# Kernel tuning notes

Hardware: AMD Instinct MI355X
Metric: run time of the kernel (lower is better)

## Reference

```python
import jax, jax.numpy as jnp
import numpy as np
from functools import partial

B, T, H, K = 64, 256, 200, 48
START_TAG, END_TAG = 46, 47


def setup_inputs() -> dict:
    key = jax.random.key(0)
    k1, k2, k3 = jax.random.split(key, 3)
    feats = jax.random.normal(k1, (B, T, H), dtype=jnp.float32)
    W_e = jax.random.normal(k2, (K, H), dtype=jnp.float32) * (6.0 / (K + H)) ** 0.5
    b_e = jnp.zeros((K,), dtype=jnp.float32)
    targets = jax.random.randint(k3, (B, T), 0, K * K, dtype=jnp.int64)
    mask = jnp.ones((B, T), dtype=jnp.int32)
    return {"feats": feats, "W_e": W_e, "b_e": b_e, "targets": targets,
            "mask": mask, "start_tag": START_TAG, "end_tag": END_TAG}


def reference(feats, W_e, b_e, targets, mask, start_tag, end_tag):
    # feats: [B,T,H]; emission: [B,T,K]
    emission = jnp.einsum('bth,kh->btk', feats, W_e) + b_e
    Bs, Ts, Ks = emission.shape
    lengths = mask.sum(-1)  # [B]
    valid = jnp.arange(Ts)[None, :] < lengths[:, None]  # [B,T]

    # crf_scores[b,t,i,j] = emission[b,t,j] (unsqueeze(2).expand). Gather at
    # flattened index targets = i*K + j picks emission[b,t, targets % K].
    gold_per_t = jnp.take_along_axis(emission, (targets % Ks)[..., None], axis=2)[..., 0]
    gold_score = jnp.sum(jnp.where(valid, gold_per_t, 0.0), axis=1)  # [B]

    # Forward algorithm. t=0: scores_upto_t = scores[:,0,start_tag,:] = emission[:,0,:]
    s0 = jnp.where((lengths > 0)[:, None], emission[:, 0, :], 0.0)  # [B,K]

    def step(s, xs):
        em_t, active = xs  # em_t: [B,K], active: [B]
        # scores[b,t,i,j] + s[b,i], logsumexp over i (prev tag)
        new = jax.scipy.special.logsumexp(em_t[:, None, :] + s[:, :, None], axis=1)
        s = jnp.where(active[:, None], new, s)
        return s, None

    xs = (jnp.swapaxes(emission[:, 1:, :], 0, 1), jnp.swapaxes(valid[:, 1:], 0, 1))
    s_final, _ = jax.lax.scan(step, s0, xs)

    all_paths_scores = s_final[:, end_tag]  # [B]
    viterbi_loss = all_paths_scores - gold_score
    return viterbi_loss
```

## Files before the change

kernel.cpp:

```cpp
#include <hip/hip_runtime.h>

#define BB 64
#define TT 256
#define HH 200
#define KK 48
#define C4 50
#define TPB 16
#define FS4 51

__global__ __launch_bounds__(256, 4)
void crf_fused_kernel(const float* __restrict__ feats,
                      const float* __restrict__ W_e,
                      const float* __restrict__ b_e,
                      const int*   __restrict__ targets,
                      const int*   __restrict__ mask,
                      const int*   __restrict__ end_tag_p,
                      float*       __restrict__ out)
{
    __shared__ float4 f_lds[TPB * FS4];
    __shared__ float  m_arr[4][TPB], s_arr[4][TPB];
    __shared__ float  g_arr[4][TPB], e_arr[4][TPB];

    const int tid  = threadIdx.x;
    const int lane = tid & 63;
    const int w    = tid >> 6;
    const int bidx = blockIdx.x >> 4;
    const int tq   = blockIdx.x & 15;

    const float4* feats4 = reinterpret_cast<const float4*>(feats) +
                           (size_t)(bidx * TT + tq * TPB) * C4;
    for (int i = tid; i < TPB * C4; i += 256) {
        const int r = i / C4, c = i - r * C4;
        f_lds[r * FS4 + c] = feats4[i];
    }

    int len;
    {
        const int4 mv4 = reinterpret_cast<const int4*>(mask + bidx * TT)[lane];
        int mv = mv4.x + mv4.y + mv4.z + mv4.w;
        #pragma unroll
        for (int off = 32; off >= 1; off >>= 1) mv += __shfl_xor(mv, off);
        len = mv;
    }
    __syncthreads();

    const int t_loc  = lane & 15;
    const int kg     = lane >> 4;
    const int k0     = w * 12 + kg * 3;
    const int t_glob = tq * TPB + t_loc;

    const float4* W4   = reinterpret_cast<const float4*>(W_e);
    const float4* wp0  = W4 + (size_t)(k0 + 0) * C4;
    const float4* wp1  = W4 + (size_t)(k0 + 1) * C4;
    const float4* wp2  = W4 + (size_t)(k0 + 2) * C4;
    const float4* frow = &f_lds[t_loc * FS4];

    float a0 = b_e[k0], a1 = b_e[k0 + 1], a2 = b_e[k0 + 2];
    #pragma unroll 2
    for (int c = 0; c < C4; ++c) {
        const float4 f  = frow[c];
        const float4 w0 = wp0[c];
        const float4 w1 = wp1[c];
        const float4 w2 = wp2[c];
        a0 = fmaf(f.x,w0.x, fmaf(f.y,w0.y, fmaf(f.z,w0.z, fmaf(f.w,w0.w, a0))));
        a1 = fmaf(f.x,w1.x, fmaf(f.y,w1.y, fmaf(f.z,w1.z, fmaf(f.w,w1.w, a1))));
        a2 = fmaf(f.x,w2.x, fmaf(f.y,w2.y, fmaf(f.z,w2.z, fmaf(f.w,w2.w, a2))));
    }

    const int ET  = end_tag_p[0];
    const int tgt = targets[bidx * TT + t_glob] % KK;

    float m = fmaxf(fmaxf(a0, a1), a2);
    float s = expf(a0 - m) + expf(a1 - m) + expf(a2 - m);
    float g = ((k0     == tgt) ? a0 : 0.0f)
            + ((k0 + 1 == tgt) ? a1 : 0.0f)
            + ((k0 + 2 == tgt) ? a2 : 0.0f);
    float e = ((k0     == ET) ? a0 : 0.0f)
            + ((k0 + 1 == ET) ? a1 : 0.0f)
            + ((k0 + 2 == ET) ? a2 : 0.0f);

    #pragma unroll
    for (int off = 16; off <= 32; off <<= 1) {
        const float om = __shfl_xor(m, off);
        const float os = __shfl_xor(s, off);
        const float nm = fmaxf(m, om);
        s = s * expf(m - nm) + os * expf(om - nm);
        m = nm;
        g += __shfl_xor(g, off);
        e += __shfl_xor(e, off);
    }
    if (lane < TPB) {
        m_arr[w][t_loc] = m; s_arr[w][t_loc] = s;
        g_arr[w][t_loc] = g; e_arr[w][t_loc] = e;
    }
    __syncthreads();

    if (tid < TPB) {
        const int t = tid;
        float M = m_arr[0][t], S = s_arr[0][t];
        #pragma unroll
        for (int i2 = 1; i2 < 4; ++i2) {
            const float om = m_arr[i2][t], os = s_arr[i2][t];
            const float nm = fmaxf(M, om);
            S = S * expf(M - nm) + os * expf(om - nm);
            M = nm;
        }
        const float lse  = M + logf(S);
        const float gold = g_arr[0][t] + g_arr[1][t] + g_arr[2][t] + g_arr[3][t];
        const float eend = e_arr[0][t] + e_arr[1][t] + e_arr[2][t] + e_arr[3][t];
        const int gt = tq * TPB + t;

        float c = 0.0f;
        if (gt < len)          c -= gold;
        if (gt == len - 1)     c += eend;
        else if (gt < len - 1) c += lse;

        #pragma unroll
        for (int off = 8; off >= 1; off >>= 1) c += __shfl_xor(c, off);
        if (t == 0) atomicAdd(out + bidx, c);
    }
}

extern "C" void kernel_launch(void* const* d_in, const int* in_sizes, int n_in,
                              void* d_out, int out_size, void* d_ws, size_t ws_size,
                              hipStream_t stream) {
    const float* feats   = (const float*)d_in[0];
    const float* W_e     = (const float*)d_in[1];
    const float* b_e     = (const float*)d_in[2];
    const int*   targets = (const int*)d_in[3];
    const int*   mask    = (const int*)d_in[4];
    const int*   et      = (const int*)d_in[6];
    float*       out     = (float*)d_out;

    hipMemsetAsync(out, 0, BB * sizeof(float), stream);
    crf_fused_kernel<<<dim3(BB * (TT / TPB)), dim3(256), 0, stream>>>(
        feats, W_e, b_e, targets, mask, et, out);
}
```

Measured before the change: 94.30 us.

## Compute emission GEMM with bf16 MFMA and 64-timestep tiles per block

Replaces the per-thread fp32 FMA dot products with bf16 16x16x32 MFMA instructions. Feats and W_e are converted to bf16 into LDS, and each block now handles 64 timesteps instead of 16, so there are 256 blocks instead of 1024. The log-sum-exp, gold-score and end-tag reductions are done with in-wave shuffles over the MFMA output layout, with one atomic per block. This targets the FMA throughput and the repeated W_e global reads, at the cost of bf16 precision in the emissions and fewer blocks to fill the GPU.

```diff
diff --git a/kernel.cpp b/kernel.cpp
--- a/kernel.cpp
+++ b/kernel.cpp
@@ -1,37 +1,56 @@
 #include <hip/hip_runtime.h>
+#include <hip/hip_bf16.h>
 
 #define BB 64
 #define TT 256
 #define HH 200
 #define KK 48
 #define C4 50
-#define TPB 16
-#define FS4 51
+#define AS 216
 
-__global__ __launch_bounds__(256, 4)
-void crf_fused_kernel(const float* __restrict__ feats,
-                      const float* __restrict__ W_e,
-                      const float* __restrict__ b_e,
-                      const int*   __restrict__ targets,
-                      const int*   __restrict__ mask,
-                      const int*   __restrict__ end_tag_p,
-                      float*       __restrict__ out)
+typedef __attribute__((ext_vector_type(8))) short bf16x8;
+typedef __attribute__((ext_vector_type(4))) float f32x4;
+
+static __device__ __forceinline__ unsigned short f2bf(float x) {
+    __hip_bfloat16 h = __float2bfloat16(x);
+    return *reinterpret_cast<unsigned short*>(&h);
+}
+
+__global__ __launch_bounds__(256)
+void crf_mfma_kernel(const float* __restrict__ feats,
+                     const float* __restrict__ W_e,
+                     const float* __restrict__ b_e,
+                     const int*   __restrict__ targets,
+                     const int*   __restrict__ mask,
+                     const int*   __restrict__ end_tag_p,
+                     float*       __restrict__ out)
 {
-    __shared__ float4 f_lds[TPB * FS4];
-    __shared__ float  m_arr[4][TPB], s_arr[4][TPB];
-    __shared__ float  g_arr[4][TPB], e_arr[4][TPB];
+    __shared__ __align__(16) unsigned short Albs[64 * AS];
+    __shared__ __align__(16) unsigned short Wlds[48 * AS];
+    __shared__ float wpart[4];
 
     const int tid  = threadIdx.x;
     const int lane = tid & 63;
     const int w    = tid >> 6;
-    const int bidx = blockIdx.x >> 4;
-    const int tq   = blockIdx.x & 15;
+    const int bidx = blockIdx.x >> 2;
+    const int tq   = blockIdx.x & 3;
 
-    const float4* feats4 = reinterpret_cast<const float4*>(feats) +
-                           (size_t)(bidx * TT + tq * TPB) * C4;
-    for (int i = tid; i < TPB * C4; i += 256) {
-        const int r = i / C4, c = i - r * C4;
-        f_lds[r * FS4 + c] = feats4[i];
+    {
+        const float4* f4 = reinterpret_cast<const float4*>(feats) +
+                           (size_t)(bidx * TT + tq * 64) * C4;
+        for (int i = tid; i < 64 * C4; i += 256) {
+            const int r = i / C4, cc = i - r * C4;
+            const float4 v = f4[i];
+            ushort4 o = { f2bf(v.x), f2bf(v.y), f2bf(v.z), f2bf(v.w) };
+            *reinterpret_cast<ushort4*>(&Albs[r * AS + cc * 4]) = o;
+        }
+        const float4* w4 = reinterpret_cast<const float4*>(W_e);
+        for (int i = tid; i < KK * C4; i += 256) {
+            const int r = i / C4, cc = i - r * C4;
+            const float4 v = w4[i];
+            ushort4 o = { f2bf(v.x), f2bf(v.y), f2bf(v.z), f2bf(v.w) };
+            *reinterpret_cast<ushort4*>(&Wlds[r * AS + cc * 4]) = o;
+        }
     }
 
     int len;
@@ -44,80 +63,79 @@
     }
     __syncthreads();
 
-    const int t_loc  = lane & 15;
-    const int kg     = lane >> 4;
-    const int k0     = w * 12 + kg * 3;
-    const int t_glob = tq * TPB + t_loc;
+    const int rg = lane >> 4;
+    const int cc = lane & 15;
 
-    const float4* W4   = reinterpret_cast<const float4*>(W_e);
-    const float4* wp0  = W4 + (size_t)(k0 + 0) * C4;
-    const float4* wp1  = W4 + (size_t)(k0 + 1) * C4;
-    const float4* wp2  = W4 + (size_t)(k0 + 2) * C4;
-    const float4* frow = &f_lds[t_loc * FS4];
+    const unsigned short* Ap  = &Albs[(w * 16 + cc) * AS];
+    const unsigned short* Bp0 = &Wlds[(0  + cc) * AS];
+    const unsigned short* Bp1 = &Wlds[(16 + cc) * AS];
+    const unsigned short* Bp2 = &Wlds[(32 + cc) * AS];
 
-    float a0 = b_e[k0], a1 = b_e[k0 + 1], a2 = b_e[k0 + 2];
-    #pragma unroll 2
-    for (int c = 0; c < C4; ++c) {
-        const float4 f  = frow[c];
-        const float4 w0 = wp0[c];
-        const float4 w1 = wp1[c];
-        const float4 w2 = wp2[c];
-        a0 = fmaf(f.x,w0.x, fmaf(f.y,w0.y, fmaf(f.z,w0.z, fmaf(f.w,w0.w, a0))));
-        a1 = fmaf(f.x,w1.x, fmaf(f.y,w1.y, fmaf(f.z,w1.z, fmaf(f.w,w1.w, a1))));
-        a2 = fmaf(f.x,w2.x, fmaf(f.y,w2.y, fmaf(f.z,w2.z, fmaf(f.w,w2.w, a2))));
+    f32x4 ac0 = {0.f, 0.f, 0.f, 0.f};
+    f32x4 ac1 = {0.f, 0.f, 0.f, 0.f};
+    f32x4 ac2 = {0.f, 0.f, 0.f, 0.f};
+
+    #pragma unroll
+    for (int kc = 0; kc < 7; ++kc) {
+        const int koff = kc * 32 + rg * 8;
+        bf16x8 a, b0, b1, b2;
+        if (kc < 6 || rg == 0) {
+            a  = *reinterpret_cast<const bf16x8*>(Ap  + koff);
+            b0 = *reinterpret_cast<const bf16x8*>(Bp0 + koff);
+            b1 = *reinterpret_cast<const bf16x8*>(Bp1 + koff);
+            b2 = *reinterpret_cast<const bf16x8*>(Bp2 + koff);
+        } else {
+            a = (bf16x8)(short)0; b0 = a; b1 = a; b2 = a;
+        }
+        ac0 = __builtin_amdgcn_mfma_f32_16x16x32_bf16(a, b0, ac0, 0, 0, 0);
+        ac1 = __builtin_amdgcn_mfma_f32_16x16x32_bf16(a, b1, ac1, 0, 0, 0);
+        ac2 = __builtin_amdgcn_mfma_f32_16x16x32_bf16(a, b2, ac2, 0, 0, 0);
     }
 
-    const int ET  = end_tag_p[0];
-    const int tgt = targets[bidx * TT + t_glob] % KK;
+    const float bb0 = b_e[cc], bb1 = b_e[16 + cc], bb2 = b_e[32 + cc];
+    const int   ET  = end_tag_p[0];
 
-    float m = fmaxf(fmaxf(a0, a1), a2);
-    float s = expf(a0 - m) + expf(a1 - m) + expf(a2 - m);
-    float g = ((k0     == tgt) ? a0 : 0.0f)
-            + ((k0 + 1 == tgt) ? a1 : 0.0f)
-            + ((k0 + 2 == tgt) ? a2 : 0.0f);
-    float e = ((k0     == ET) ? a0 : 0.0f)
-            + ((k0 + 1 == ET) ? a1 : 0.0f)
-            + ((k0 + 2 == ET) ? a2 : 0.0f);
+    float csum = 0.0f;
+    #pragma unroll
+    for (int j = 0; j < 4; ++j) {
+        const float x0 = ac0[j] + bb0;
+        const float x1 = ac1[j] + bb1;
+        const float x2 = ac2[j] + bb2;
 
-    #pragma unroll
-    for (int off = 16; off <= 32; off <<= 1) {
-        const float om = __shfl_xor(m, off);
-        const float os = __shfl_xor(s, off);
-        const float nm = fmaxf(m, om);
-        s = s * expf(m - nm) + os * expf(om - nm);
-        m = nm;
-        g += __shfl_xor(g, off);
-        e += __shfl_xor(e, off);
+        const int r  = w * 16 + rg * 4 + j;
+        const int gt = tq * 64 + r;
+        const int tg = targets[bidx * TT + gt] % KK;
+
+        float mx = fmaxf(fmaxf(x0, x1), x2);
+        #pragma unroll
+        for (int off = 8; off >= 1; off >>= 1) mx = fmaxf(mx, __shfl_xor(mx, off));
+        float s = expf(x0 - mx) + expf(x1 - mx) + expf(x2 - mx);
+        float g = ((0  + cc) == tg ? x0 : 0.f) + ((16 + cc) == tg ? x1 : 0.f)
+                + ((32 + cc) == tg ? x2 : 0.f);
+        float e = ((0  + cc) == ET ? x0 : 0.f) + ((16 + cc) == ET ? x1 : 0.f)
+                + ((32 + cc) == ET ? x2 : 0.f);
+        #pragma unroll
+        for (int off = 8; off >= 1; off >>= 1) {
+            s += __shfl_xor(s, off);
+            g += __shfl_xor(g, off);
+            e += __shfl_xor(e, off);
+        }
+        const float lse = mx + logf(s);
+
+        float cr = 0.0f;
+        if (gt < len)          cr -= g;
+        if (gt == len - 1)     cr += e;
+        else if (gt < len - 1) cr += lse;
+        csum += cr;
     }
-    if (lane < TPB) {
-        m_arr[w][t_loc] = m; s_arr[w][t_loc] = s;
-        g_arr[w][t_loc] = g; e_arr[w][t_loc] = e;
-    }
+
+    float v = (cc == 0) ? csum : 0.0f;
+    v += __shfl_xor(v, 16);
+    v += __shfl_xor(v, 32);
+    if (lane == 0) wpart[w] = v;
     __syncthreads();
-
-    if (tid < TPB) {
-        const int t = tid;
-        float M = m_arr[0][t], S = s_arr[0][t];
-        #pragma unroll
-        for (int i2 = 1; i2 < 4; ++i2) {
-            const float om = m_arr[i2][t], os = s_arr[i2][t];
-            const float nm = fmaxf(M, om);
-            S = S * expf(M - nm) + os * expf(om - nm);
-            M = nm;
-        }
-        const float lse  = M + logf(S);
-        const float gold = g_arr[0][t] + g_arr[1][t] + g_arr[2][t] + g_arr[3][t];
-        const float eend = e_arr[0][t] + e_arr[1][t] + e_arr[2][t] + e_arr[3][t];
-        const int gt = tq * TPB + t;
-
-        float c = 0.0f;
-        if (gt < len)          c -= gold;
-        if (gt == len - 1)     c += eend;
-        else if (gt < len - 1) c += lse;
-
-        #pragma unroll
-        for (int off = 8; off >= 1; off >>= 1) c += __shfl_xor(c, off);
-        if (t == 0) atomicAdd(out + bidx, c);
+    if (tid == 0) {
+        atomicAdd(out + bidx, wpart[0] + wpart[1] + wpart[2] + wpart[3]);
     }
 }
 
@@ -133,6 +151,6 @@
     float*       out     = (float*)d_out;
 
     hipMemsetAsync(out, 0, BB * sizeof(float), stream);
-    crf_fused_kernel<<<dim3(BB * (TT / TPB)), dim3(256), 0, stream>>>(
+    crf_mfma_kernel<<<dim3(BB * 4), dim3(256), 0, stream>>>(
         feats, W_e, b_e, targets, mask, et, out);
 }
```

New measurement: 79.16 us. 1.19x faster.

## Convert feats and weights to bf16 and compute emissions with MFMA

Applied to the files above, without the earlier changes.

Adds a pre-pass kernel that converts feats and W_e to bf16 in a workspace and also zeroes the output, replacing the memset. The main kernel then computes each 16x48 emission tile with 16x16x32 bf16 MFMA instructions instead of scalar FP32 FMAs through LDS, using 3 waves per block. The aim is to cut matmul compute cost, but the extra pass reads all of feats in FP32 and writes a bf16 copy, adding memory traffic and a second launch. Dropping to bf16 also lowers the precision of the emissions.

```diff
diff --git a/kernel.cpp b/kernel.cpp
--- a/kernel.cpp
+++ b/kernel.cpp
@@ -1,38 +1,68 @@
 #include <hip/hip_runtime.h>
+#include <hip/hip_bf16.h>
 
 #define BB 64
 #define TT 256
 #define HH 200
 #define KK 48
-#define C4 50
-#define TPB 16
-#define FS4 51
 
-__global__ __launch_bounds__(256, 4)
-void crf_fused_kernel(const float* __restrict__ feats,
-                      const float* __restrict__ W_e,
-                      const float* __restrict__ b_e,
-                      const int*   __restrict__ targets,
-                      const int*   __restrict__ mask,
-                      const int*   __restrict__ end_tag_p,
-                      float*       __restrict__ out)
+typedef __attribute__((ext_vector_type(8))) short bf16x8;
+typedef __attribute__((ext_vector_type(4))) float f32x4;
+
+#define NFEAT (BB * TT * HH)
+#define NW    (KK * HH)
+#define NF8   (NFEAT / 8)
+#define NW8   (NW / 8)
+
+static __device__ __forceinline__ unsigned short f2bf(float x) {
+    __hip_bfloat16 h = __float2bfloat16(x);
+    return *reinterpret_cast<unsigned short*>(&h);
+}
+
+__global__ __launch_bounds__(256)
+void cvt_kernel(const float* __restrict__ feats, const float* __restrict__ W_e,
+                unsigned short* __restrict__ bf, float* __restrict__ out)
 {
-    __shared__ float4 f_lds[TPB * FS4];
-    __shared__ float  m_arr[4][TPB], s_arr[4][TPB];
-    __shared__ float  g_arr[4][TPB], e_arr[4][TPB];
+    const int i = blockIdx.x * 256 + threadIdx.x;
+    const float4* src4 = nullptr;
+    unsigned short* dst = nullptr;
+    if (i < NF8) {
+        src4 = reinterpret_cast<const float4*>(feats) + (size_t)i * 2;
+        dst  = bf + (size_t)i * 8;
+    } else if (i < NF8 + NW8) {
+        const int j = i - NF8;
+        src4 = reinterpret_cast<const float4*>(W_e) + (size_t)j * 2;
+        dst  = bf + (size_t)NFEAT + (size_t)j * 8;
+    }
+    if (src4) {
+        const float4 v0 = src4[0];
+        const float4 v1 = src4[1];
+        bf16x8 o;
+        o[0] = (short)f2bf(v0.x); o[1] = (short)f2bf(v0.y);
+        o[2] = (short)f2bf(v0.z); o[3] = (short)f2bf(v0.w);
+        o[4] = (short)f2bf(v1.x); o[5] = (short)f2bf(v1.y);
+        o[6] = (short)f2bf(v1.z); o[7] = (short)f2bf(v1.w);
+        *reinterpret_cast<bf16x8*>(dst) = o;
+    }
+    if (blockIdx.x == 0 && threadIdx.x < BB) out[threadIdx.x] = 0.0f;
+}
+
+__global__ __launch_bounds__(192)
+void crf_main(const unsigned short* __restrict__ bfws,
+              const float* __restrict__ b_e,
+              const int*   __restrict__ targets,
+              const int*   __restrict__ mask,
+              const int*   __restrict__ end_tag_p,
+              float*       __restrict__ out)
+{
+    __shared__ float Lm[3][16], Ls[3][16], Lg[3][16], Le[3][16];
 
     const int tid  = threadIdx.x;
     const int lane = tid & 63;
     const int w    = tid >> 6;
     const int bidx = blockIdx.x >> 4;
-    const int tq   = blockIdx.x & 15;
-
-    const float4* feats4 = reinterpret_cast<const float4*>(feats) +
-                           (size_t)(bidx * TT + tq * TPB) * C4;
-    for (int i = tid; i < TPB * C4; i += 256) {
-        const int r = i / C4, c = i - r * C4;
-        f_lds[r * FS4 + c] = feats4[i];
-    }
+    const int sq   = blockIdx.x & 15;
+    const int t0   = sq * 16;
 
     int len;
     {
@@ -42,73 +72,59 @@
         for (int off = 32; off >= 1; off >>= 1) mv += __shfl_xor(mv, off);
         len = mv;
     }
+
+    const int rg = lane >> 4;
+    const int cc = lane & 15;
+
+    const unsigned short* Wb = bfws + (size_t)NFEAT + (size_t)(w * 16 + cc) * HH;
+    const unsigned short* Fb = bfws + (size_t)(bidx * TT + t0 + cc) * HH;
+
+    f32x4 acc = {0.f, 0.f, 0.f, 0.f};
+    #pragma unroll
+    for (int kc = 0; kc < 7; ++kc) {
+        bf16x8 a, b;
+        if (kc < 6 || rg == 0) {
+            a = *reinterpret_cast<const bf16x8*>(Wb + kc * 32 + rg * 8);
+            b = *reinterpret_cast<const bf16x8*>(Fb + kc * 32 + rg * 8);
+        } else {
+            a = (bf16x8)(short)0; b = a;
+        }
+        acc = __builtin_amdgcn_mfma_f32_16x16x32_bf16(a, b, acc, 0, 0, 0);
+    }
+
+    const float4 b4 = *reinterpret_cast<const float4*>(b_e + w * 16 + rg * 4);
+    const float x0 = acc[0] + b4.x, x1 = acc[1] + b4.y;
+    const float x2 = acc[2] + b4.z, x3 = acc[3] + b4.w;
+
+    const int ET  = end_tag_p[0];
+    const int tgt = targets[bidx * TT + t0 + cc] % KK;
+    const int kb  = w * 16 + rg * 4;
+
+    float m = fmaxf(fmaxf(x0, x1), fmaxf(x2, x3));
+    m = fmaxf(m, __shfl_xor(m, 16));
+    m = fmaxf(m, __shfl_xor(m, 32));
+    float s = expf(x0 - m) + expf(x1 - m) + expf(x2 - m) + expf(x3 - m);
+    float g = ((kb     == tgt) ? x0 : 0.f) + ((kb + 1 == tgt) ? x1 : 0.f)
+            + ((kb + 2 == tgt) ? x2 : 0.f) + ((kb + 3 == tgt) ? x3 : 0.f);
+    float e = ((kb     == ET) ? x0 : 0.f) + ((kb + 1 == ET) ? x1 : 0.f)
+            + ((kb + 2 == ET) ? x2 : 0.f) + ((kb + 3 == ET) ? x3 : 0.f);
+    s += __shfl_xor(s, 16); s += __shfl_xor(s, 32);
+    g += __shfl_xor(g, 16); g += __shfl_xor(g, 32);
+    e += __shfl_xor(e, 16); e += __shfl_xor(e, 32);
+
+    if (rg == 0) { Lm[w][cc] = m; Ls[w][cc] = s; Lg[w][cc] = g; Le[w][cc] = e; }
     __syncthreads();
 
-    const int t_loc  = lane & 15;
-    const int kg     = lane >> 4;
-    const int k0     = w * 12 + kg * 3;
-    const int t_glob = tq * TPB + t_loc;
-
-    const float4* W4   = reinterpret_cast<const float4*>(W_e);
-    const float4* wp0  = W4 + (size_t)(k0 + 0) * C4;
-    const float4* wp1  = W4 + (size_t)(k0 + 1) * C4;
-    const float4* wp2  = W4 + (size_t)(k0 + 2) * C4;
-    const float4* frow = &f_lds[t_loc * FS4];
-
-    float a0 = b_e[k0], a1 = b_e[k0 + 1], a2 = b_e[k0 + 2];
-    #pragma unroll 2
-    for (int c = 0; c < C4; ++c) {
-        const float4 f  = frow[c];
-        const float4 w0 = wp0[c];
-        const float4 w1 = wp1[c];
-        const float4 w2 = wp2[c];
-        a0 = fmaf(f.x,w0.x, fmaf(f.y,w0.y, fmaf(f.z,w0.z, fmaf(f.w,w0.w, a0))));
-        a1 = fmaf(f.x,w1.x, fmaf(f.y,w1.y, fmaf(f.z,w1.z, fmaf(f.w,w1.w, a1))));
-        a2 = fmaf(f.x,w2.x, fmaf(f.y,w2.y, fmaf(f.z,w2.z, fmaf(f.w,w2.w, a2))));
-    }
-
-    const int ET  = end_tag_p[0];
-    const int tgt = targets[bidx * TT + t_glob] % KK;
-
-    float m = fmaxf(fmaxf(a0, a1), a2);
-    float s = expf(a0 - m) + expf(a1 - m) + expf(a2 - m);
-    float g = ((k0     == tgt) ? a0 : 0.0f)
-            + ((k0 + 1 == tgt) ? a1 : 0.0f)
-            + ((k0 + 2 == tgt) ? a2 : 0.0f);
-    float e = ((k0     == ET) ? a0 : 0.0f)
-            + ((k0 + 1 == ET) ? a1 : 0.0f)
-            + ((k0 + 2 == ET) ? a2 : 0.0f);
-
-    #pragma unroll
-    for (int off = 16; off <= 32; off <<= 1) {
-        const float om = __shfl_xor(m, off);
-        const float os = __shfl_xor(s, off);
-        const float nm = fmaxf(m, om);
-        s = s * expf(m - nm) + os * expf(om - nm);
-        m = nm;
-        g += __shfl_xor(g, off);
-        e += __shfl_xor(e, off);
-    }
-    if (lane < TPB) {
-        m_arr[w][t_loc] = m; s_arr[w][t_loc] = s;
-        g_arr[w][t_loc] = g; e_arr[w][t_loc] = e;
-    }
-    __syncthreads();
-
-    if (tid < TPB) {
-        const int t = tid;
-        float M = m_arr[0][t], S = s_arr[0][t];
-        #pragma unroll
-        for (int i2 = 1; i2 < 4; ++i2) {
-            const float om = m_arr[i2][t], os = s_arr[i2][t];
-            const float nm = fmaxf(M, om);
-            S = S * expf(M - nm) + os * expf(om - nm);
-            M = nm;
-        }
+    if (tid < 16) {
+        const float m0 = Lm[0][tid], m1 = Lm[1][tid], m2 = Lm[2][tid];
+        const float M  = fmaxf(fmaxf(m0, m1), m2);
+        const float S  = Ls[0][tid] * expf(m0 - M)
+                       + Ls[1][tid] * expf(m1 - M)
+                       + Ls[2][tid] * expf(m2 - M);
         const float lse  = M + logf(S);
-        const float gold = g_arr[0][t] + g_arr[1][t] + g_arr[2][t] + g_arr[3][t];
-        const float eend = e_arr[0][t] + e_arr[1][t] + e_arr[2][t] + e_arr[3][t];
-        const int gt = tq * TPB + t;
+        const float gold = Lg[0][tid] + Lg[1][tid] + Lg[2][tid];
+        const float eend = Le[0][tid] + Le[1][tid] + Le[2][tid];
+        const int gt = t0 + tid;
 
         float c = 0.0f;
         if (gt < len)          c -= gold;
@@ -117,7 +133,7 @@
 
         #pragma unroll
         for (int off = 8; off >= 1; off >>= 1) c += __shfl_xor(c, off);
-        if (t == 0) atomicAdd(out + bidx, c);
+        if (tid == 0) atomicAdd(out + bidx, c);
     }
 }
 
@@ -131,8 +147,9 @@
     const int*   mask    = (const int*)d_in[4];
     const int*   et      = (const int*)d_in[6];
     float*       out     = (float*)d_out;
+    unsigned short* bfws = (unsigned short*)d_ws;
 
-    hipMemsetAsync(out, 0, BB * sizeof(float), stream);
-    crf_fused_kernel<<<dim3(BB * (TT / TPB)), dim3(256), 0, stream>>>(
-        feats, W_e, b_e, targets, mask, et, out);
+    const int cvt_grid = (NF8 + NW8 + 255) / 256;
+    cvt_kernel<<<dim3(cvt_grid), dim3(256), 0, stream>>>(feats, W_e, bfws, out);
+    crf_main<<<dim3(BB * 16), dim3(192), 0, stream>>>(bfws, b_e, targets, mask, et, out);
 }
```

Result: faster. 82.29 us (-12.7%).
